# Kernel tuning notes

Hardware: AMD Instinct MI355X
Metric: run time of the kernel (lower is better)

The kernel has to match this reference:

```python
import jax, jax.numpy as jnp
import numpy as np

N, E, IN_F, OUT_F, H = 15000, 720000, 256, 128, 4
NEG_SLOPE = 0.2

def setup_inputs() -> dict:
    key = jax.random.key(0)
    k1, k2, k3, k4, k5 = jax.random.split(key, 5)
    x = jax.random.normal(k1, (N, IN_F), jnp.float32)
    # xavier_uniform with gain=1.414 -> scale sqrt(6/(fan_in+fan_out))*gain; approximate with scaled normal-magnitude uniform
    w_bound = 1.414 * np.sqrt(6.0 / (IN_F + OUT_F))
    a_bound = 1.414 * np.sqrt(6.0 / (2 * OUT_F + 1))
    W = jax.random.uniform(k2, (H, IN_F, OUT_F), jnp.float32, -w_bound, w_bound)
    a = jax.random.uniform(k3, (H, 2 * OUT_F, 1), jnp.float32, -a_bound, a_bound)
    src = jax.random.randint(k4, (E,), 0, N, jnp.int32)
    dst = jax.random.randint(k5, (E,), 0, N, jnp.int32)
    edge_index = jnp.stack([src, dst], axis=0)  # [2, E]
    return {"x": x, "W": W, "a": a, "edge_index": edge_index}

def reference(x, W, a, edge_index):
    num_nodes = x.shape[0]
    out_f = W.shape[2]
    # [H, N, O]
    x_t = jnp.einsum('ni,hio->hno', x, W)
    src, dst = edge_index[0], edge_index[1]
    # cat([x_src, x_dst], -1) @ a  ==  x_src @ a[:, :O] + x_dst @ a[:, O:]
    s_src = jnp.einsum('hno,ho->hn', x_t, a[:, :out_f, 0])  # [H, N]
    s_dst = jnp.einsum('hno,ho->hn', x_t, a[:, out_f:, 0])  # [H, N]
    e = jax.nn.leaky_relu(s_src[:, src] + s_dst[:, dst], NEG_SLOPE)  # [H, E]
    # per-head max over edges, matching e[h].max() in the source
    w = jnp.exp(e - jnp.max(e, axis=1, keepdims=True))  # [H, E]
    denom = jnp.zeros((w.shape[0], num_nodes), w.dtype).at[:, dst].add(w)  # [H, N]
    alpha = w / (denom[:, dst] + 1e-16)  # [H, E] normalized attention per edge
    # FAITHFUL to torch.einsum('hnn,hno->hno', attention, x_t): repeated 'n' in one
    # operand extracts the DIAGONAL of the dense attention matrix, so only
    # self-loop edges (src == dst) contribute: out[h,n,:] = attn[h,n,n] * x_t[h,n,:]
    self_alpha = jnp.where(src == dst, alpha, 0.0)  # [H, E]
    diag = jnp.zeros((w.shape[0], num_nodes), w.dtype).at[:, src].add(self_alpha)  # [H, N]
    out = diag[:, :, None] * x_t  # [H, N, O]
    # concat=True -> [N, H*O]
    return out.transpose(1, 0, 2).reshape(num_nodes, -1)
```

## Files before the change

kernel.cpp:

```cpp
#include <hip/hip_runtime.h>
#include <hip/hip_bf16.h>

#define HH 4
#define INF 256
#define OUTF 128
#define NEG_SLOPE 0.2f
#define LIST_CAP 8192

__global__ void k_prep(const float* __restrict__ W, const float* __restrict__ a,
                       const int* __restrict__ src, const int* __restrict__ dst, int E,
                       float* __restrict__ u, int* __restrict__ flag,
                       int* __restrict__ count, int* __restrict__ list) {
    if (blockIdx.x < 8) {
        int c = blockIdx.x, kind = c >> 2, h = c & 3;
        __shared__ float av[OUTF];
        int t = threadIdx.x;
        if (t < OUTF) av[t] = a[h * 2 * OUTF + kind * OUTF + t];
        __syncthreads();
        const float* Wr = W + ((size_t)(h * INF + t)) * OUTF;
        float acc = 0.f;
        #pragma unroll 8
        for (int o = 0; o < OUTF; ++o) acc += Wr[o] * av[o];
        u[c * INF + t] = acc;
    } else {
        int e = (blockIdx.x - 8) * blockDim.x + threadIdx.x;
        if (e < E) {
            int s = src[e], d = dst[e];
            if (s == d) {
                flag[s] = 1;
                int pos = atomicAdd(count, 1);
                if (pos < LIST_CAP) list[pos] = e;
            }
        }
    }
}

__global__ void k_s(const float* __restrict__ x, const float* __restrict__ u,
                    float4* __restrict__ s_src, float4* __restrict__ s_dst, int N) {
    __shared__ float uL[8][INF];
    for (int i = threadIdx.x; i < 8 * INF; i += blockDim.x)
        uL[i >> 8][i & 255] = u[i];
    __syncthreads();
    int wave = threadIdx.x >> 6, lane = threadIdx.x & 63;
    int n = blockIdx.x * 4 + wave;
    if (n >= N) return;
    float4 xv4 = *(const float4*)(x + (size_t)n * INF + lane * 4);
    float xv[4] = {xv4.x, xv4.y, xv4.z, xv4.w};
    float p[8];
    #pragma unroll
    for (int c = 0; c < 8; ++c) {
        float acc = 0.f;
        #pragma unroll
        for (int j = 0; j < 4; ++j) acc += xv[j] * uL[c][lane * 4 + j];
        p[c] = acc;
    }
    #pragma unroll
    for (int c = 0; c < 8; ++c)
        #pragma unroll
        for (int off = 32; off; off >>= 1) p[c] += __shfl_down(p[c], off, 64);
    if (lane == 0) {
        s_src[n] = make_float4(p[0], p[1], p[2], p[3]);
        s_dst[n] = make_float4(p[4], p[5], p[6], p[7]);
    }
}

__global__ void k_denom(const int* __restrict__ src, const int* __restrict__ dst, int E,
                        const int* __restrict__ flag,
                        const float4* __restrict__ s_src, const float4* __restrict__ s_dst,
                        float* __restrict__ denom, float* __restrict__ wsum) {
    int e = blockIdx.x * blockDim.x + threadIdx.x;
    if (e >= E) return;
    int d = dst[e];
    if (!flag[d]) return;
    int s = src[e];
    float4 sa = s_src[s], sb = s_dst[d];
    float eh[4] = {sa.x + sb.x, sa.y + sb.y, sa.z + sb.z, sa.w + sb.w};
    bool selfe = (s == d);
    #pragma unroll
    for (int h = 0; h < 4; ++h) {
        float z = eh[h];
        z = z > 0.f ? z : NEG_SLOPE * z;
        float w = expf(z);
        atomicAdd(&denom[d * 4 + h], w);
        if (selfe) atomicAdd(&wsum[d * 4 + h], w);
    }
}

__global__ void k_out(const float* __restrict__ x, const float* __restrict__ W,
                      const int* __restrict__ src,
                      const int* __restrict__ count, const int* __restrict__ list,
                      const float* __restrict__ denom, const float* __restrict__ wsum,
                      float* __restrict__ out) {
    int cnt = *count;
    if (cnt > LIST_CAP) cnt = LIST_CAP;
    __shared__ float xL[INF];
    for (int idx = blockIdx.x; idx < cnt; idx += gridDim.x) {
        int e = list[idx];
        int n = src[e];
        __syncthreads();
        for (int t = threadIdx.x; t < INF; t += blockDim.x)
            xL[t] = x[(size_t)n * INF + t];
        __syncthreads();
        int t = threadIdx.x;
        int h = t >> 7, o = t & 127;
        float dg = wsum[n * 4 + h] / (denom[n * 4 + h] + 1e-16f);
        const float* Wc = W + (size_t)h * INF * OUTF + o;
        float acc = 0.f;
        #pragma unroll 8
        for (int i = 0; i < INF; ++i) acc += xL[i] * Wc[(size_t)i * OUTF];
        out[(size_t)n * (HH * OUTF) + h * OUTF + o] = dg * acc;
    }
}

extern "C" void kernel_launch(void* const* d_in, const int* in_sizes, int n_in,
                              void* d_out, int out_size, void* d_ws, size_t ws_size,
                              hipStream_t stream) {
    const float* x = (const float*)d_in[0];
    const float* W = (const float*)d_in[1];
    const float* a = (const float*)d_in[2];
    const int* ei = (const int*)d_in[3];
    int N = in_sizes[0] / INF;
    int E = in_sizes[3] / 2;
    const int* src = ei;
    const int* dst = ei + E;

    char* ws = (char*)d_ws;
    float*  u     = (float*)ws;
    float4* ssrc  = (float4*)(ws + 8192);
    float4* sdst  = (float4*)(ws + 8192 + (size_t)N * 16);
    size_t zoff   = 8192 + (size_t)N * 32;
    float*  denom = (float*)(ws + zoff);
    float*  wsum  = (float*)(ws + zoff + (size_t)N * 16);
    int*    flag  = (int*)  (ws + zoff + (size_t)N * 32);
    int*    count = (int*)  (ws + zoff + (size_t)N * 36);
    int*    list  = count + 1;
    size_t zbytes = (size_t)N * 36 + 4;

    hipMemsetAsync(ws + zoff, 0, zbytes, stream);
    hipMemsetAsync(d_out, 0, (size_t)out_size * sizeof(float), stream);

    int eblocks = (E + 255) / 256;
    k_prep<<<8 + eblocks, 256, 0, stream>>>(W, a, src, dst, E, u, flag, count, list);
    k_s<<<(N + 3) / 4, 256, 0, stream>>>(x, u, ssrc, sdst, N);
    k_denom<<<eblocks, 256, 0, stream>>>(src, dst, E, flag, ssrc, sdst, denom, wsum);
    k_out<<<128, 512, 0, stream>>>(x, W, src, count, list, denom, wsum, (float*)d_out);
}
```

Measured before the change: 52.88 us.

## Replace memsets with kernel zeroing, fuse scan into score kernel, write output per node

Both hipMemsetAsync calls go away. Workspace zeroing moves into the first kernel, and the self-loop flag scan is fused into the score kernel, which removes the atomic list and counter. The output kernel now walks every node. It writes zeros for nodes with zero self-weight and computes the projection for the rest with two outputs per thread, so the separate 30 MB output memset is no longer needed. The trade-off is a sweep over all nodes in the output kernel and a zero test on wsum in place of the flag, which is inexact if a self-loop weight underflows to zero.

```diff
diff --git a/kernel.cpp b/kernel.cpp
--- a/kernel.cpp
+++ b/kernel.cpp
@@ -1,16 +1,12 @@
 #include <hip/hip_runtime.h>
-#include <hip/hip_bf16.h>
 
 #define HH 4
 #define INF 256
 #define OUTF 128
 #define NEG_SLOPE 0.2f
-#define LIST_CAP 8192
 
-__global__ void k_prep(const float* __restrict__ W, const float* __restrict__ a,
-                       const int* __restrict__ src, const int* __restrict__ dst, int E,
-                       float* __restrict__ u, int* __restrict__ flag,
-                       int* __restrict__ count, int* __restrict__ list) {
+__global__ void k1_init(const float* __restrict__ W, const float* __restrict__ a,
+                        float* __restrict__ u, float4* __restrict__ zbase, int zquads) {
     if (blockIdx.x < 8) {
         int c = blockIdx.x, kind = c >> 2, h = c & 3;
         __shared__ float av[OUTF];
@@ -23,51 +19,55 @@
         for (int o = 0; o < OUTF; ++o) acc += Wr[o] * av[o];
         u[c * INF + t] = acc;
     } else {
-        int e = (blockIdx.x - 8) * blockDim.x + threadIdx.x;
+        int i = (blockIdx.x - 8) * blockDim.x + threadIdx.x;
+        if (i < zquads) zbase[i] = make_float4(0.f, 0.f, 0.f, 0.f);
+    }
+}
+
+__global__ void k2_s_scan(const float* __restrict__ x, const float* __restrict__ u,
+                          const int* __restrict__ src, const int* __restrict__ dst,
+                          int N, int E, int sBlocks,
+                          float4* __restrict__ s_src, float4* __restrict__ s_dst,
+                          int* __restrict__ flag) {
+    if (blockIdx.x < sBlocks) {
+        __shared__ float uL[8][INF];
+        for (int i = threadIdx.x; i < 8 * INF; i += blockDim.x)
+            uL[i >> 8][i & 255] = u[i];
+        __syncthreads();
+        int wave = threadIdx.x >> 6, lane = threadIdx.x & 63;
+        int n = blockIdx.x * 4 + wave;
+        if (n >= N) return;
+        float4 xv4 = *(const float4*)(x + (size_t)n * INF + lane * 4);
+        float xv[4] = {xv4.x, xv4.y, xv4.z, xv4.w};
+        float p[8];
+        #pragma unroll
+        for (int c = 0; c < 8; ++c) {
+            float acc = 0.f;
+            #pragma unroll
+            for (int j = 0; j < 4; ++j) acc += xv[j] * uL[c][lane * 4 + j];
+            p[c] = acc;
+        }
+        #pragma unroll
+        for (int c = 0; c < 8; ++c)
+            #pragma unroll
+            for (int off = 32; off; off >>= 1) p[c] += __shfl_down(p[c], off, 64);
+        if (lane == 0) {
+            s_src[n] = make_float4(p[0], p[1], p[2], p[3]);
+            s_dst[n] = make_float4(p[4], p[5], p[6], p[7]);
+        }
+    } else {
+        int e = (blockIdx.x - sBlocks) * blockDim.x + threadIdx.x;
         if (e < E) {
-            int s = src[e], d = dst[e];
-            if (s == d) {
-                flag[s] = 1;
-                int pos = atomicAdd(count, 1);
-                if (pos < LIST_CAP) list[pos] = e;
-            }
+            int s = src[e];
+            if (s == dst[e]) flag[s] = 1;
         }
     }
 }
 
-__global__ void k_s(const float* __restrict__ x, const float* __restrict__ u,
-                    float4* __restrict__ s_src, float4* __restrict__ s_dst, int N) {
-    __shared__ float uL[8][INF];
-    for (int i = threadIdx.x; i < 8 * INF; i += blockDim.x)
-        uL[i >> 8][i & 255] = u[i];
-    __syncthreads();
-    int wave = threadIdx.x >> 6, lane = threadIdx.x & 63;
-    int n = blockIdx.x * 4 + wave;
-    if (n >= N) return;
-    float4 xv4 = *(const float4*)(x + (size_t)n * INF + lane * 4);
-    float xv[4] = {xv4.x, xv4.y, xv4.z, xv4.w};
-    float p[8];
-    #pragma unroll
-    for (int c = 0; c < 8; ++c) {
-        float acc = 0.f;
-        #pragma unroll
-        for (int j = 0; j < 4; ++j) acc += xv[j] * uL[c][lane * 4 + j];
-        p[c] = acc;
-    }
-    #pragma unroll
-    for (int c = 0; c < 8; ++c)
-        #pragma unroll
-        for (int off = 32; off; off >>= 1) p[c] += __shfl_down(p[c], off, 64);
-    if (lane == 0) {
-        s_src[n] = make_float4(p[0], p[1], p[2], p[3]);
-        s_dst[n] = make_float4(p[4], p[5], p[6], p[7]);
-    }
-}
-
-__global__ void k_denom(const int* __restrict__ src, const int* __restrict__ dst, int E,
-                        const int* __restrict__ flag,
-                        const float4* __restrict__ s_src, const float4* __restrict__ s_dst,
-                        float* __restrict__ denom, float* __restrict__ wsum) {
+__global__ void k3_denom(const int* __restrict__ src, const int* __restrict__ dst, int E,
+                         const int* __restrict__ flag,
+                         const float4* __restrict__ s_src, const float4* __restrict__ s_dst,
+                         float* __restrict__ denom, float* __restrict__ wsum) {
     int e = blockIdx.x * blockDim.x + threadIdx.x;
     if (e >= E) return;
     int d = dst[e];
@@ -86,29 +86,38 @@
     }
 }
 
-__global__ void k_out(const float* __restrict__ x, const float* __restrict__ W,
-                      const int* __restrict__ src,
-                      const int* __restrict__ count, const int* __restrict__ list,
-                      const float* __restrict__ denom, const float* __restrict__ wsum,
-                      float* __restrict__ out) {
-    int cnt = *count;
-    if (cnt > LIST_CAP) cnt = LIST_CAP;
+__global__ __launch_bounds__(256)
+void k4_out(const float* __restrict__ x, const float* __restrict__ W,
+            const float* __restrict__ denom, const float* __restrict__ wsum,
+            float2* __restrict__ out2, int N, int nodesPerBlock) {
     __shared__ float xL[INF];
-    for (int idx = blockIdx.x; idx < cnt; idx += gridDim.x) {
-        int e = list[idx];
-        int n = src[e];
-        __syncthreads();
-        for (int t = threadIdx.x; t < INF; t += blockDim.x)
+    int n0 = blockIdx.x * nodesPerBlock;
+    int n1 = n0 + nodesPerBlock; if (n1 > N) n1 = N;
+    int t = threadIdx.x;
+    for (int n = n0; n < n1; ++n) {
+        float4 wv = *(const float4*)(wsum + (size_t)n * 4);
+        bool flg = (wv.x != 0.f) | (wv.y != 0.f) | (wv.z != 0.f) | (wv.w != 0.f);
+        if (flg) {
+            float4 dv = *(const float4*)(denom + (size_t)n * 4);
+            float d0 = wv.x / (dv.x + 1e-16f), d1 = wv.y / (dv.y + 1e-16f);
+            float d2 = wv.z / (dv.z + 1e-16f), d3 = wv.w / (dv.w + 1e-16f);
+            __syncthreads();
             xL[t] = x[(size_t)n * INF + t];
-        __syncthreads();
-        int t = threadIdx.x;
-        int h = t >> 7, o = t & 127;
-        float dg = wsum[n * 4 + h] / (denom[n * 4 + h] + 1e-16f);
-        const float* Wc = W + (size_t)h * INF * OUTF + o;
-        float acc = 0.f;
-        #pragma unroll 8
-        for (int i = 0; i < INF; ++i) acc += xL[i] * Wc[(size_t)i * OUTF];
-        out[(size_t)n * (HH * OUTF) + h * OUTF + o] = dg * acc;
+            __syncthreads();
+            int j = 2 * t, h = t >> 6, o = j & 127;
+            float dg = (h == 0) ? d0 : (h == 1) ? d1 : (h == 2) ? d2 : d3;
+            const float* Wc = W + (size_t)h * INF * OUTF + o;
+            float acc0 = 0.f, acc1 = 0.f;
+            #pragma unroll 8
+            for (int i = 0; i < INF; ++i) {
+                float xi = xL[i];
+                acc0 += xi * Wc[(size_t)i * OUTF];
+                acc1 += xi * Wc[(size_t)i * OUTF + 1];
+            }
+            out2[(size_t)n * 256 + t] = make_float2(dg * acc0, dg * acc1);
+        } else {
+            out2[(size_t)n * 256 + t] = make_float2(0.f, 0.f);
+        }
     }
 }
 
@@ -125,23 +134,26 @@
     const int* dst = ei + E;
 
     char* ws = (char*)d_ws;
-    float*  u     = (float*)ws;
-    float4* ssrc  = (float4*)(ws + 8192);
-    float4* sdst  = (float4*)(ws + 8192 + (size_t)N * 16);
-    size_t zoff   = 8192 + (size_t)N * 32;
+    float*  u    = (float*)ws;
+    float4* ssrc = (float4*)(ws + 8192);
+    float4* sdst = (float4*)(ws + 8192 + (size_t)N * 16);
+    size_t zoff  = 8192 + (size_t)N * 32;
     float*  denom = (float*)(ws + zoff);
     float*  wsum  = (float*)(ws + zoff + (size_t)N * 16);
     int*    flag  = (int*)  (ws + zoff + (size_t)N * 32);
-    int*    count = (int*)  (ws + zoff + (size_t)N * 36);
-    int*    list  = count + 1;
-    size_t zbytes = (size_t)N * 36 + 4;
+    size_t zbytes = (size_t)N * 36;
+    int zquads = (int)((zbytes + 15) / 16);
 
-    hipMemsetAsync(ws + zoff, 0, zbytes, stream);
-    hipMemsetAsync(d_out, 0, (size_t)out_size * sizeof(float), stream);
+    int zblocks = (zquads + 255) / 256;
+    k1_init<<<8 + zblocks, 256, 0, stream>>>(W, a, u, (float4*)(ws + zoff), zquads);
 
-    int eblocks = (E + 255) / 256;
-    k_prep<<<8 + eblocks, 256, 0, stream>>>(W, a, src, dst, E, u, flag, count, list);
-    k_s<<<(N + 3) / 4, 256, 0, stream>>>(x, u, ssrc, sdst, N);
-    k_denom<<<eblocks, 256, 0, stream>>>(src, dst, E, flag, ssrc, sdst, denom, wsum);
-    k_out<<<128, 512, 0, stream>>>(x, W, src, count, list, denom, wsum, (float*)d_out);
+    int sBlocks = (N + 3) / 4;
+    int eBlocks = (E + 255) / 256;
+    k2_s_scan<<<sBlocks + eBlocks, 256, 0, stream>>>(x, u, src, dst, N, E, sBlocks,
+                                                     ssrc, sdst, flag);
+    k3_denom<<<eBlocks, 256, 0, stream>>>(src, dst, E, flag, ssrc, sdst, denom, wsum);
+
+    int nodesPerBlock = 8;
+    int oBlocks = (N + nodesPerBlock - 1) / nodesPerBlock;
+    k4_out<<<oBlocks, 256, 0, stream>>>(x, W, denom, wsum, (float2*)d_out, N, nodesPerBlock);
 }
```

Result: slower. 56.56 us (+7.0%).
